# Optimization experiments

Hardware: AMD Instinct MI355X
Metric: run time of the kernel (lower is better)

The kernel has to match this reference:

```python
import jax, jax.numpy as jnp
import numpy as np

N_NODES = 50000
N_EDGES = 800000
IN_DIM = 128
HID = 256
OUT_DIM = 256
N_HEADS = 8
E_DIM = 64
KV_IN = 2 * IN_DIM + E_DIM  # 320


def _mlp_params(key, din, dhid, dout):
    k1, k2 = jax.random.split(key)
    s1 = 1.0 / np.sqrt(din)
    s2 = 1.0 / np.sqrt(dhid)
    return (jax.random.uniform(k1, (din, dhid), jnp.float32, -s1, s1),
            jnp.zeros((dhid,), jnp.float32),
            jax.random.uniform(k2, (dhid, dout), jnp.float32, -s2, s2),
            jnp.zeros((dout,), jnp.float32))


def setup_inputs() -> dict:
    key = jax.random.key(0)
    kh, ke, kidx, kk, kv, kq = jax.random.split(key, 6)
    h = jax.random.normal(kh, (N_NODES, IN_DIM), jnp.float32)
    e = jax.random.normal(ke, (N_EDGES, E_DIM), jnp.float32)
    edge_index = jax.random.randint(kidx, (2, N_EDGES), 0, N_NODES, jnp.int64)
    Wk1, bk1, Wk2, bk2 = _mlp_params(kk, KV_IN, HID, OUT_DIM)
    Wv1, bv1, Wv2, bv2 = _mlp_params(kv, KV_IN, HID, OUT_DIM)
    Wq1, bq1, Wq2, bq2 = _mlp_params(kq, IN_DIM, HID, OUT_DIM)
    return {"h": h, "e": e, "edge_index": edge_index,
            "Wk1": Wk1, "bk1": bk1, "Wk2": Wk2, "bk2": bk2,
            "Wv1": Wv1, "bv1": bv1, "Wv2": Wv2, "bv2": bv2,
            "Wq1": Wq1, "bq1": bq1, "Wq2": Wq2, "bq2": bq2}


def _mlp(x, W1, b1, W2, b2):
    # MLP(in, out, hidden, norm=False): Linear -> ReLU -> Linear
    return jax.nn.relu(x @ W1 + b1) @ W2 + b2


def reference(h, e, edge_index,
              Wk1, bk1, Wk2, bk2,
              Wv1, bv1, Wv2, bv2,
              Wq1, bq1, Wq2, bq2):
    N = h.shape[0]
    d_head = OUT_DIM // N_HEADS
    src, dst = edge_index[0], edge_index[1]
    # gather endpoints: hi = h[dst], hj = h[src]
    kv_input = jnp.concatenate([e, h[dst], h[src]], axis=-1)  # [E, KV_IN]
    k = _mlp(kv_input, Wk1, bk1, Wk2, bk2).reshape(-1, N_HEADS, d_head)
    v = _mlp(kv_input, Wv1, bv1, Wv2, bv2).reshape(-1, N_HEADS, d_head)
    q = _mlp(h, Wq1, bq1, Wq2, bq2).reshape(-1, N_HEADS, d_head)
    # per-edge logits, scaled dot product [E, H]
    logits = jnp.sum(q[dst] * k, axis=-1) * (1.0 / np.sqrt(d_head))
    # scatter softmax over destination groups
    mx = jax.ops.segment_max(logits, dst, num_segments=N)  # [N, H]
    ex = jnp.exp(logits - mx[dst])
    den = jax.ops.segment_sum(ex, dst, num_segments=N)  # [N, H]
    alpha = ex / den[dst]  # [E, H]
    # weighted scatter-sum aggregate
    m = alpha[..., None] * v  # [E, H, d_head]
    out = jax.ops.segment_sum(m, dst, num_segments=N)  # [N, H, d_head]
    return out.reshape(N, OUT_DIM)
```

## Files before the change

### kernel.cpp

```cpp
#include <hip/hip_runtime.h>

#define NND 50000
#define NE  800000
#define IND 128
#define HD  256
#define OD  256
#define NH  8
#define ED  64

typedef __attribute__((ext_vector_type(8))) short bf16x8;
typedef __attribute__((ext_vector_type(4))) float f32x4;

__device__ __forceinline__ float bf2f(unsigned short u) {
    union { unsigned int i; float f; } x; x.i = ((unsigned int)u) << 16; return x.f;
}
__device__ __forceinline__ unsigned short f2bf(float f) {
    union { float f; unsigned int i; } x; x.f = f;
    unsigned int u = x.i;
    u += 0x7FFFu + ((u >> 16) & 1u);
    return (unsigned short)(u >> 16);
}
__device__ __forceinline__ unsigned int pk2(float a, float b) {
    return (unsigned int)f2bf(a) | ((unsigned int)f2bf(b) << 16);
}

__global__ void k_hist(const int* __restrict__ eidx, int* __restrict__ cnt) {
    int e = blockIdx.x * 256 + threadIdx.x;
    if (e < NE) atomicAdd(&cnt[eidx[NE + e]], 1);
}

__global__ __launch_bounds__(1024) void k_scan(const int* __restrict__ cnt,
                                               int* __restrict__ head) {
    __shared__ int part[1024];
    const int t = threadIdx.x;
    const int CH = (NND + 1023) / 1024;
    int base = t * CH;
    int s = 0;
    for (int i = 0; i < CH; ++i) { int idx = base + i; if (idx < NND) s += cnt[idx]; }
    part[t] = s;
    __syncthreads();
    for (int off = 1; off < 1024; off <<= 1) {
        int v = (t >= off) ? part[t - off] : 0;
        __syncthreads();
        part[t] += v;
        __syncthreads();
    }
    int excl = (t == 0) ? 0 : part[t - 1];
    for (int i = 0; i < CH; ++i) {
        int idx = base + i; if (idx >= NND) break;
        head[idx] = excl;
        excl += cnt[idx];
    }
}

__global__ void k_scatter(const int* __restrict__ eidx, int* __restrict__ head,
                          int* __restrict__ perm, int* __restrict__ srcS,
                          int* __restrict__ dstS) {
    int e = blockIdx.x * 256 + threadIdx.x;
    if (e < NE) {
        int s = eidx[e];
        int d = eidx[NE + e];
        int pos = atomicAdd(&head[d], 1);
        perm[pos] = e;
        srcS[pos] = s;
        dstS[pos] = d;
    }
}

__global__ void k_eperm(const float* __restrict__ eattr, const int* __restrict__ perm,
                        unsigned short* __restrict__ ebf) {
    int i = blockIdx.x * 256 + threadIdx.x;
    if (i >= NE * 16) return;
    int pos = i >> 4, j = i & 15;
    int eid = perm[pos];
    float4 v = *(const float4*)(eattr + (size_t)eid * ED + j * 4);
    ushort4 o; o.x = f2bf(v.x); o.y = f2bf(v.y); o.z = f2bf(v.z); o.w = f2bf(v.w);
    *(ushort4*)(ebf + (size_t)pos * ED + j * 4) = o;
}

__global__ void k_packw(const float* __restrict__ W, unsigned short* __restrict__ P,
                        int K, int N, int rowoff) {
    int tid = blockIdx.x * 256 + threadIdx.x;
    if (tid >= K * N) return;
    int j = tid & 7;
    int l = (tid >> 3) & 63;
    int rest = tid >> 9;
    int KS = K >> 5;
    int ks = rest % KS;
    int ct = rest / KS;
    int n = ct * 16 + (l & 15);
    int k = ks * 32 + (l >> 4) * 8 + j;
    P[tid] = f2bf(W[(size_t)(rowoff + k) * N + n]);
}

__device__ __forceinline__ void zero_acc(f32x4 (&acc)[4][4]) {
    #pragma unroll
    for (int c = 0; c < 4; ++c)
        #pragma unroll
        for (int i = 0; i < 4; ++i)
            #pragma unroll
            for (int r = 0; r < 4; ++r) acc[c][i][r] = 0.f;
}

template<int KS, int STRIDE>
__device__ __forceinline__ void gemmT(const unsigned short* X,
                                      const unsigned short* __restrict__ Wp,
                                      int w, int l, f32x4 (&acc)[4][4]) {
    for (int ks = 0; ks < KS; ++ks) {
        bf16x8 wf[4], xf[4];
        #pragma unroll
        for (int c = 0; c < 4; ++c)
            wf[c] = *(const bf16x8*)(Wp + (((4 * w + c) * KS + ks) * 64 + l) * 8);
        #pragma unroll
        for (int i = 0; i < 4; ++i)
            xf[i] = *(const bf16x8*)(X + (i * 16 + (l & 15)) * STRIDE + ks * 32 + (l >> 4) * 8);
        #pragma unroll
        for (int c = 0; c < 4; ++c)
            #pragma unroll
            for (int i = 0; i < 4; ++i)
                acc[c][i] = __builtin_amdgcn_mfma_f32_16x16x32_bf16(wf[c], xf[i], acc[c][i], 0, 0, 0);
    }
}

__device__ __forceinline__ void lin_epi(const unsigned short* __restrict__ Wp,
                                        unsigned short* __restrict__ outp,
                                        const unsigned short* sXp,
                                        int w, int l, int g, int el, int m0) {
    f32x4 acc[4][4];
    zero_acc(acc);
    gemmT<4, 136>(sXp, Wp, w, l, acc);
    #pragma unroll
    for (int c = 0; c < 4; ++c) {
        int hid0 = 64 * w + 16 * c + 4 * g;
        #pragma unroll
        for (int i = 0; i < 4; ++i) {
            int node = m0 + 16 * i + el;
            if (node < NND) {
                uint2 pk;
                pk.x = pk2(acc[c][i][0], acc[c][i][1]);
                pk.y = pk2(acc[c][i][2], acc[c][i][3]);
                *(uint2*)(outp + (size_t)node * HD + hid0) = pk;
            }
        }
    }
}

__global__ __launch_bounds__(256) void k_node(
    const float* __restrict__ h,
    const unsigned short* __restrict__ Wq1p, const float* __restrict__ bq1,
    const unsigned short* __restrict__ Wq2p, const float* __restrict__ bq2,
    unsigned short* __restrict__ qb,
    const unsigned short* __restrict__ WdK, const unsigned short* __restrict__ WsK,
    const unsigned short* __restrict__ WdV, const unsigned short* __restrict__ WsV,
    unsigned short* __restrict__ udK, unsigned short* __restrict__ usK,
    unsigned short* __restrict__ udV, unsigned short* __restrict__ usV)
{
    __shared__ unsigned short sX[64][136];
    __shared__ unsigned short sH[64][264];
    const int t = threadIdx.x, w = t >> 6, l = t & 63;
    const int g = l >> 4, el = l & 15;
    const int m0 = blockIdx.x * 64;

    for (int c = t; c < 2048; c += 256) {
        int row = c >> 5, j = c & 31;
        int node = m0 + row; if (node >= NND) node = NND - 1;
        float4 v = *(const float4*)(h + (size_t)node * IND + j * 4);
        ushort4 o; o.x = f2bf(v.x); o.y = f2bf(v.y); o.z = f2bf(v.z); o.w = f2bf(v.w);
        *(ushort4*)(&sX[row][j * 4]) = o;
    }
    __syncthreads();

    f32x4 acc[4][4];
    zero_acc(acc);
    gemmT<4, 136>(&sX[0][0], Wq1p, w, l, acc);
    #pragma unroll
    for (int c = 0; c < 4; ++c) {
        int hid0 = 64 * w + 16 * c + 4 * g;
        float4 bv = *(const float4*)(bq1 + hid0);
        #pragma unroll
        for (int i = 0; i < 4; ++i) {
            uint2 pk;
            pk.x = pk2(fmaxf(acc[c][i][0] + bv.x, 0.f), fmaxf(acc[c][i][1] + bv.y, 0.f));
            pk.y = pk2(fmaxf(acc[c][i][2] + bv.z, 0.f), fmaxf(acc[c][i][3] + bv.w, 0.f));
            *(uint2*)(&sH[16 * i + el][hid0]) = pk;
        }
    }
    __syncthreads();

    zero_acc(acc);
    gemmT<8, 264>(&sH[0][0], Wq2p, w, l, acc);
    #pragma unroll
    for (int c = 0; c < 4; ++c) {
        int out0 = 64 * w + 16 * c + 4 * g;
        float4 bv = *(const float4*)(bq2 + out0);
        #pragma unroll
        for (int i = 0; i < 4; ++i) {
            int node = m0 + 16 * i + el;
            if (node < NND) {
                uint2 pk;
                pk.x = pk2(acc[c][i][0] + bv.x, acc[c][i][1] + bv.y);
                pk.y = pk2(acc[c][i][2] + bv.z, acc[c][i][3] + bv.w);
                *(uint2*)(qb + (size_t)node * OD + out0) = pk;
            }
        }
    }

    lin_epi(WdK, udK, &sX[0][0], w, l, g, el, m0);
    lin_epi(WsK, usK, &sX[0][0], w, l, g, el, m0);
    lin_epi(WdV, udV, &sX[0][0], w, l, g, el, m0);
    lin_epi(WsV, usV, &sX[0][0], w, l, g, el, m0);
}

struct SmF {
    unsigned short E[64][72];
    unsigned short H[64][264];
    int   Src[64];
    int   Dst[64];
    float Ex[64][8];
};

__device__ __forceinline__ void epi_pre(SmF& sm, f32x4 (&acc)[4][4],
                                        const float* __restrict__ b1,
                                        int w, int g, int el) {
    #pragma unroll
    for (int c = 0; c < 4; ++c) {
        int hid0 = 64 * w + 16 * c + 4 * g;
        float4 bv = *(const float4*)(b1 + hid0);
        #pragma unroll
        for (int i = 0; i < 4; ++i) {
            uint2 pk;
            pk.x = pk2(acc[c][i][0] + bv.x, acc[c][i][1] + bv.y);
            pk.y = pk2(acc[c][i][2] + bv.z, acc[c][i][3] + bv.w);
            *(uint2*)(&sm.H[16 * i + el][hid0]) = pk;
        }
    }
}

__device__ __forceinline__ void elemwise(SmF& sm,
                                         const unsigned short* __restrict__ ud,
                                         const unsigned short* __restrict__ us,
                                         int t) {
    int er = t >> 2;
    const unsigned short* udr = ud + (size_t)sm.Dst[er] * HD;
    const unsigned short* usr = us + (size_t)sm.Src[er] * HD;
    bf16x8 vd[8], vs[8];
    #pragma unroll
    for (int j = 0; j < 8; ++j) {
        int col = (j * 4 + (t & 3)) * 8;
        vd[j] = *(const bf16x8*)(udr + col);
        vs[j] = *(const bf16x8*)(usr + col);
    }
    #pragma unroll
    for (int j = 0; j < 8; ++j) {
        int col = (j * 4 + (t & 3)) * 8;
        bf16x8 hv = *(const bf16x8*)(&sm.H[er][col]);
        bf16x8 o;
        #pragma unroll
        for (int u = 0; u < 8; ++u) {
            float x = bf2f((unsigned short)hv[u]) + bf2f((unsigned short)vd[j][u])
                    + bf2f((unsigned short)vs[j][u]);
            o[u] = (short)f2bf(x > 0.f ? x : 0.f);
        }
        *(bf16x8*)(&sm.H[er][col]) = o;
    }
}

template<int PRE>
__global__ __launch_bounds__(256, 3) void k_edgeF(
    const float* __restrict__ eattr, const unsigned short* __restrict__ ebf,
    const int* __restrict__ perm,
    const int* __restrict__ srcS, const int* __restrict__ dstS,
    const unsigned short* __restrict__ WeK, const float* __restrict__ b1K,
    const unsigned short* __restrict__ W2K, const float* __restrict__ b2K,
    const unsigned short* __restrict__ WeV, const float* __restrict__ b1V,
    const unsigned short* __restrict__ W2V, const float* __restrict__ b2V,
    const unsigned short* __restrict__ udK, const unsigned short* __restrict__ usK,
    const unsigned short* __restrict__ udV, const unsigned short* __restrict__ usV,
    const unsigned short* __restrict__ qb,
    float* __restrict__ den, float* __restrict__ outp)
{
    __shared__ SmF sm;
    const int t = threadIdx.x, w = t >> 6, l = t & 63;
    const int g = l >> 4, el = l & 15;
    const int e0 = blockIdx.x * 64;

    if (t < 64) { sm.Src[t] = srcS[e0 + t]; sm.Dst[t] = dstS[e0 + t]; }
    if (PRE) {
        for (int c = t; c < 512; c += 256) {
            int row = c >> 3, j = c & 7;
            *(bf16x8*)(&sm.E[row][j * 8]) =
                *(const bf16x8*)(ebf + (size_t)(e0 + row) * ED + j * 8);
        }
    } else {
        for (int c = t; c < 1024; c += 256) {
            int row = c >> 4, j = c & 15;
            int eid = perm[e0 + row];
            float4 v = *(const float4*)(eattr + (size_t)eid * ED + j * 4);
            ushort4 o; o.x = f2bf(v.x); o.y = f2bf(v.y); o.z = f2bf(v.z); o.w = f2bf(v.w);
            *(ushort4*)(&sm.E[row][j * 4]) = o;
        }
    }
    __syncthreads();

    f32x4 acc[4][4];

    zero_acc(acc);
    gemmT<2, 72>(&sm.E[0][0], WeK, w, l, acc);
    epi_pre(sm, acc, b1K, w, g, el);
    __syncthreads();
    elemwise(sm, udK, usK, t);
    __syncthreads();

    zero_acc(acc);
    gemmT<8, 264>(&sm.H[0][0], W2K, w, l, acc);
    __syncthreads();
    epi_pre(sm, acc, b2K, w, g, el);
    __syncthreads();

    const float scale = 0.17677669529663687f;
    for (int p = t; p < 512; p += 256) {
        int er = p >> 3, hh = p & 7;
        const unsigned short* qrow = qb + (size_t)sm.Dst[er] * OD + hh * 32;
        float s = 0.f;
        #pragma unroll
        for (int jj = 0; jj < 32; jj += 8) {
            bf16x8 qv = *(const bf16x8*)(qrow + jj);
            bf16x8 kv = *(const bf16x8*)(&sm.H[er][hh * 32 + jj]);
            #pragma unroll
            for (int u = 0; u < 8; ++u)
                s += bf2f((unsigned short)qv[u]) * bf2f((unsigned short)kv[u]);
        }
        sm.Ex[er][hh] = __expf(s * scale);
    }
    __syncthreads();
    if (t < NH) {
        float run = 0.f; int prev = sm.Dst[0];
        for (int er = 0; er < 64; ++er) {
            int dn = sm.Dst[er];
            if (dn != prev) { atomicAdd(&den[prev * NH + t], run); run = 0.f; prev = dn; }
            run += sm.Ex[er][t];
        }
        atomicAdd(&den[prev * NH + t], run);
    }
    __syncthreads();

    zero_acc(acc);
    gemmT<2, 72>(&sm.E[0][0], WeV, w, l, acc);
    epi_pre(sm, acc, b1V, w, g, el);
    __syncthreads();
    elemwise(sm, udV, usV, t);
    __syncthreads();

    zero_acc(acc);
    gemmT<8, 264>(&sm.H[0][0], W2V, w, l, acc);
    __syncthreads();

    #pragma unroll
    for (int c = 0; c < 4; ++c) {
        int out0 = 64 * w + 16 * c + 4 * g;
        float4 bv = *(const float4*)(b2V + out0);
        int hh = out0 >> 5;
        #pragma unroll
        for (int i = 0; i < 4; ++i) {
            int edge = 16 * i + el;
            float ex = sm.Ex[edge][hh];
            uint2 pk;
            pk.x = pk2((acc[c][i][0] + bv.x) * ex, (acc[c][i][1] + bv.y) * ex);
            pk.y = pk2((acc[c][i][2] + bv.z) * ex, (acc[c][i][3] + bv.w) * ex);
            *(uint2*)(&sm.H[edge][out0]) = pk;
        }
    }
    __syncthreads();

    {
        float run = 0.f; int prev = sm.Dst[0];
        for (int er = 0; er < 64; ++er) {
            int dn = sm.Dst[er];
            if (dn != prev) {
                atomicAdd(outp + (size_t)prev * OD + t, run);
                run = 0.f; prev = dn;
            }
            run += bf2f(sm.H[er][t]);
        }
        atomicAdd(outp + (size_t)prev * OD + t, run);
    }
}

__global__ void k_norm(float* __restrict__ outp, const float* __restrict__ den) {
    int i = blockIdx.x * 256 + threadIdx.x;
    if (i >= NND * OD / 4) return;
    int node = i >> 6;
    int c4 = i & 63;
    int hh = (c4 >> 3);
    float inv = 1.f / den[node * NH + hh];
    float4 v = *(float4*)(outp + (size_t)i * 4);
    v.x *= inv; v.y *= inv; v.z *= inv; v.w *= inv;
    *(float4*)(outp + (size_t)i * 4) = v;
}

extern "C" void kernel_launch(void* const* d_in, const int* in_sizes, int n_in,
                              void* d_out, int out_size, void* d_ws, size_t ws_size,
                              hipStream_t stream)
{
    const float* h   = (const float*)d_in[0];
    const float* e   = (const float*)d_in[1];
    const int*   eid = (const int*)  d_in[2];
    const float* Wk1 = (const float*)d_in[3];
    const float* bk1 = (const float*)d_in[4];
    const float* Wk2 = (const float*)d_in[5];
    const float* bk2 = (const float*)d_in[6];
    const float* Wv1 = (const float*)d_in[7];
    const float* bv1 = (const float*)d_in[8];
    const float* Wv2 = (const float*)d_in[9];
    const float* bv2 = (const float*)d_in[10];
    const float* Wq1 = (const float*)d_in[11];
    const float* bq1 = (const float*)d_in[12];
    const float* Wq2 = (const float*)d_in[13];
    const float* bq2 = (const float*)d_in[14];

    char* ws = (char*)d_ws;
    size_t off = 0;
    auto take = [&](size_t bytes) { char* p = ws + off; off += bytes; return p; };
    unsigned short* qb   = (unsigned short*)take(25600000);
    unsigned short* udK  = (unsigned short*)take(25600000);
    unsigned short* usK  = (unsigned short*)take(25600000);
    unsigned short* udV  = (unsigned short*)take(25600000);
    unsigned short* usV  = (unsigned short*)take(25600000);
    float*          den  = (float*)         take(1600000);
    int*            cnt  = (int*)           take(200000);
    int*            head = (int*)           take(200000);
    int*            perm = (int*)           take(3200000);
    int*            srcS = (int*)           take(3200000);
    int*            dstS = (int*)           take(3200000);
    unsigned short* Wq1p = (unsigned short*)take(65536);
    unsigned short* Wq2p = (unsigned short*)take(131072);
    unsigned short* WeK  = (unsigned short*)take(32768);
    unsigned short* W2K  = (unsigned short*)take(131072);
    unsigned short* WdK  = (unsigned short*)take(65536);
    unsigned short* WsK  = (unsigned short*)take(65536);
    unsigned short* WeV  = (unsigned short*)take(32768);
    unsigned short* W2V  = (unsigned short*)take(131072);
    unsigned short* WdV  = (unsigned short*)take(65536);
    unsigned short* WsV  = (unsigned short*)take(65536);
    const size_t needed_small = off;
    unsigned short* ebf  = (unsigned short*)take((size_t)NE * ED * 2);
    const size_t needed_full = off;

    if (ws_size < needed_small) return;
    const bool pre = (ws_size >= needed_full);

    hipMemsetAsync(d_out, 0, (size_t)NND * OD * sizeof(float), stream);
    hipMemsetAsync(den, 0, (size_t)NND * NH * sizeof(float), stream);
    hipMemsetAsync(cnt, 0, (size_t)NND * sizeof(int), stream);

    k_hist<<<(NE + 255) / 256, 256, 0, stream>>>(eid, cnt);
    k_scan<<<1, 1024, 0, stream>>>(cnt, head);
    k_scatter<<<(NE + 255) / 256, 256, 0, stream>>>(eid, head, perm, srcS, dstS);

    k_packw<<<(IND * HD + 255) / 256, 256, 0, stream>>>(Wq1, Wq1p, IND, HD, 0);
    k_packw<<<(HD * OD + 255) / 256, 256, 0, stream>>>(Wq2, Wq2p, HD, OD, 0);
    k_packw<<<(ED * HD + 255) / 256, 256, 0, stream>>>(Wk1, WeK, ED, HD, 0);
    k_packw<<<(HD * OD + 255) / 256, 256, 0, stream>>>(Wk2, W2K, HD, OD, 0);
    k_packw<<<(IND * HD + 255) / 256, 256, 0, stream>>>(Wk1, WdK, IND, HD, 64);
    k_packw<<<(IND * HD + 255) / 256, 256, 0, stream>>>(Wk1, WsK, IND, HD, 192);
    k_packw<<<(ED * HD + 255) / 256, 256, 0, stream>>>(Wv1, WeV, ED, HD, 0);
    k_packw<<<(HD * OD + 255) / 256, 256, 0, stream>>>(Wv2, W2V, HD, OD, 0);
    k_packw<<<(IND * HD + 255) / 256, 256, 0, stream>>>(Wv1, WdV, IND, HD, 64);
    k_packw<<<(IND * HD + 255) / 256, 256, 0, stream>>>(Wv1, WsV, IND, HD, 192);

    if (pre)
        k_eperm<<<(NE * 16 + 255) / 256, 256, 0, stream>>>(e, perm, ebf);

    k_node<<<(NND + 63) / 64, 256, 0, stream>>>(h, Wq1p, bq1, Wq2p, bq2, qb,
                                                WdK, WsK, WdV, WsV,
                                                udK, usK, udV, usV);

    if (pre)
        k_edgeF<1><<<NE / 64, 256, 0, stream>>>(e, ebf, perm, srcS, dstS,
                                                WeK, bk1, W2K, bk2,
                                                WeV, bv1, W2V, bv2,
                                                udK, usK, udV, usV,
                                                qb, den, (float*)d_out);
    else
        k_edgeF<0><<<NE / 64, 256, 0, stream>>>(e, ebf, perm, srcS, dstS,
                                                WeK, bk1, W2K, bk2,
                                                WeV, bv1, W2V, bv2,
                                                udK, usK, udV, usV,
                                                qb, den, (float*)d_out);

    k_norm<<<(NND * OD / 4 + 255) / 256, 256, 0, stream>>>((float*)d_out, den);
}
```

Baseline: 902.5 us.

## Drop edge-attr pre-permute kernel, use hardware bf16 pack, repad LDS strides

Removes the separate k_eperm pass and always gathers edge attributes in fp32 inside the edge kernel, converting them to bf16 in-kernel. Edge ids are staged in shared memory first, which adds one barrier. Float-to-bf16 packing now uses the v_cvt_pk_bf16_f32 instruction instead of a software rounding sequence. LDS row strides change from 72/136/264 to 80/144/272 elements, presumably to alter bank-conflict behaviour. The norm kernel also guards against zero denominators.

Measured after the change: 861.0 us. 4.6% less time.

```diff
diff --git a/kernel.cpp b/kernel.cpp
--- a/kernel.cpp
+++ b/kernel.cpp
@@ -21,7 +21,9 @@
     return (unsigned short)(u >> 16);
 }
 __device__ __forceinline__ unsigned int pk2(float a, float b) {
-    return (unsigned int)f2bf(a) | ((unsigned int)f2bf(b) << 16);
+    unsigned int r;
+    asm("v_cvt_pk_bf16_f32 %0, %1, %2" : "=v"(r) : "v"(a), "v"(b));
+    return r;
 }
 
 __global__ void k_hist(const int* __restrict__ eidx, int* __restrict__ cnt) {
@@ -65,17 +67,6 @@
         srcS[pos] = s;
         dstS[pos] = d;
     }
-}
-
-__global__ void k_eperm(const float* __restrict__ eattr, const int* __restrict__ perm,
-                        unsigned short* __restrict__ ebf) {
-    int i = blockIdx.x * 256 + threadIdx.x;
-    if (i >= NE * 16) return;
-    int pos = i >> 4, j = i & 15;
-    int eid = perm[pos];
-    float4 v = *(const float4*)(eattr + (size_t)eid * ED + j * 4);
-    ushort4 o; o.x = f2bf(v.x); o.y = f2bf(v.y); o.z = f2bf(v.z); o.w = f2bf(v.w);
-    *(ushort4*)(ebf + (size_t)pos * ED + j * 4) = o;
 }
 
 __global__ void k_packw(const float* __restrict__ W, unsigned short* __restrict__ P,
@@ -128,7 +119,7 @@
                                         int w, int l, int g, int el, int m0) {
     f32x4 acc[4][4];
     zero_acc(acc);
-    gemmT<4, 136>(sXp, Wp, w, l, acc);
+    gemmT<4, 144>(sXp, Wp, w, l, acc);
     #pragma unroll
     for (int c = 0; c < 4; ++c) {
         int hid0 = 64 * w + 16 * c + 4 * g;
@@ -155,8 +146,8 @@
     unsigned short* __restrict__ udK, unsigned short* __restrict__ usK,
     unsigned short* __restrict__ udV, unsigned short* __restrict__ usV)
 {
-    __shared__ unsigned short sX[64][136];
-    __shared__ unsigned short sH[64][264];
+    __shared__ unsigned short sX[64][144];
+    __shared__ unsigned short sH[64][272];
     const int t = threadIdx.x, w = t >> 6, l = t & 63;
     const int g = l >> 4, el = l & 15;
     const int m0 = blockIdx.x * 64;
@@ -165,14 +156,14 @@
         int row = c >> 5, j = c & 31;
         int node = m0 + row; if (node >= NND) node = NND - 1;
         float4 v = *(const float4*)(h + (size_t)node * IND + j * 4);
-        ushort4 o; o.x = f2bf(v.x); o.y = f2bf(v.y); o.z = f2bf(v.z); o.w = f2bf(v.w);
-        *(ushort4*)(&sX[row][j * 4]) = o;
+        uint2 pk; pk.x = pk2(v.x, v.y); pk.y = pk2(v.z, v.w);
+        *(uint2*)(&sX[row][j * 4]) = pk;
     }
     __syncthreads();
 
     f32x4 acc[4][4];
     zero_acc(acc);
-    gemmT<4, 136>(&sX[0][0], Wq1p, w, l, acc);
+    gemmT<4, 144>(&sX[0][0], Wq1p, w, l, acc);
     #pragma unroll
     for (int c = 0; c < 4; ++c) {
         int hid0 = 64 * w + 16 * c + 4 * g;
@@ -188,7 +179,7 @@
     __syncthreads();
 
     zero_acc(acc);
-    gemmT<8, 264>(&sH[0][0], Wq2p, w, l, acc);
+    gemmT<8, 272>(&sH[0][0], Wq2p, w, l, acc);
     #pragma unroll
     for (int c = 0; c < 4; ++c) {
         int out0 = 64 * w + 16 * c + 4 * g;
@@ -212,8 +203,9 @@
 }
 
 struct SmF {
-    unsigned short E[64][72];
-    unsigned short H[64][264];
+    unsigned short E[64][80];
+    unsigned short H[64][272];
+    int   Eid[64];
     int   Src[64];
     int   Dst[64];
     float Ex[64][8];
@@ -254,20 +246,22 @@
     for (int j = 0; j < 8; ++j) {
         int col = (j * 4 + (t & 3)) * 8;
         bf16x8 hv = *(const bf16x8*)(&sm.H[er][col]);
-        bf16x8 o;
+        float x[8];
         #pragma unroll
         for (int u = 0; u < 8; ++u) {
-            float x = bf2f((unsigned short)hv[u]) + bf2f((unsigned short)vd[j][u])
-                    + bf2f((unsigned short)vs[j][u]);
-            o[u] = (short)f2bf(x > 0.f ? x : 0.f);
-        }
-        *(bf16x8*)(&sm.H[er][col]) = o;
-    }
-}
-
-template<int PRE>
+            x[u] = bf2f((unsigned short)hv[u]) + bf2f((unsigned short)vd[j][u])
+                 + bf2f((unsigned short)vs[j][u]);
+            x[u] = fmaxf(x[u], 0.f);
+        }
+        uint4 o;
+        o.x = pk2(x[0], x[1]); o.y = pk2(x[2], x[3]);
+        o.z = pk2(x[4], x[5]); o.w = pk2(x[6], x[7]);
+        *(uint4*)(&sm.H[er][col]) = o;
+    }
+}
+
 __global__ __launch_bounds__(256, 3) void k_edgeF(
-    const float* __restrict__ eattr, const unsigned short* __restrict__ ebf,
+    const float* __restrict__ eattr,
     const int* __restrict__ perm,
     const int* __restrict__ srcS, const int* __restrict__ dstS,
     const unsigned short* __restrict__ WeK, const float* __restrict__ b1K,
@@ -284,35 +278,31 @@
     const int g = l >> 4, el = l & 15;
     const int e0 = blockIdx.x * 64;
 
-    if (t < 64) { sm.Src[t] = srcS[e0 + t]; sm.Dst[t] = dstS[e0 + t]; }
-    if (PRE) {
-        for (int c = t; c < 512; c += 256) {
-            int row = c >> 3, j = c & 7;
-            *(bf16x8*)(&sm.E[row][j * 8]) =
-                *(const bf16x8*)(ebf + (size_t)(e0 + row) * ED + j * 8);
-        }
-    } else {
-        for (int c = t; c < 1024; c += 256) {
-            int row = c >> 4, j = c & 15;
-            int eid = perm[e0 + row];
-            float4 v = *(const float4*)(eattr + (size_t)eid * ED + j * 4);
-            ushort4 o; o.x = f2bf(v.x); o.y = f2bf(v.y); o.z = f2bf(v.z); o.w = f2bf(v.w);
-            *(ushort4*)(&sm.E[row][j * 4]) = o;
-        }
+    if (t < 64) {
+        sm.Eid[t] = perm[e0 + t];
+        sm.Src[t] = srcS[e0 + t];
+        sm.Dst[t] = dstS[e0 + t];
+    }
+    __syncthreads();
+    for (int c = t; c < 1024; c += 256) {
+        int row = c >> 4, j = c & 15;
+        float4 v = *(const float4*)(eattr + (size_t)sm.Eid[row] * ED + j * 4);
+        uint2 pk; pk.x = pk2(v.x, v.y); pk.y = pk2(v.z, v.w);
+        *(uint2*)(&sm.E[row][j * 4]) = pk;
     }
     __syncthreads();
 
     f32x4 acc[4][4];
 
     zero_acc(acc);
-    gemmT<2, 72>(&sm.E[0][0], WeK, w, l, acc);
+    gemmT<2, 80>(&sm.E[0][0], WeK, w, l, acc);
     epi_pre(sm, acc, b1K, w, g, el);
     __syncthreads();
     elemwise(sm, udK, usK, t);
     __syncthreads();
 
     zero_acc(acc);
-    gemmT<8, 264>(&sm.H[0][0], W2K, w, l, acc);
+    gemmT<8, 272>(&sm.H[0][0], W2K, w, l, acc);
     __syncthreads();
     epi_pre(sm, acc, b2K, w, g, el);
     __syncthreads();
@@ -345,14 +335,14 @@
     __syncthreads();
 
     zero_acc(acc);
-    gemmT<2, 72>(&sm.E[0][0], WeV, w, l, acc);
+    gemmT<2, 80>(&sm.E[0][0], WeV, w, l, acc);
     epi_pre(sm, acc, b1V, w, g, el);
     __syncthreads();
     elemwise(sm, udV, usV, t);
     __syncthreads();
 
     zero_acc(acc);
-    gemmT<8, 264>(&sm.H[0][0], W2V, w, l, acc);
+    gemmT<8, 272>(&sm.H[0][0], W2V, w, l, acc);
     __syncthreads();
 
     #pragma unroll
@@ -392,7 +382,8 @@
     int node = i >> 6;
     int c4 = i & 63;
     int hh = (c4 >> 3);
-    float inv = 1.f / den[node * NH + hh];
+    float d = den[node * NH + hh];
+    float inv = d > 0.f ? 1.f / d : 0.f;
     float4 v = *(float4*)(outp + (size_t)i * 4);
     v.x *= inv; v.y *= inv; v.z *= inv; v.w *= inv;
     *(float4*)(outp + (size_t)i * 4) = v;
@@ -442,12 +433,8 @@
     unsigned short* W2V  = (unsigned short*)take(131072);
     unsigned short* WdV  = (unsigned short*)take(65536);
     unsigned short* WsV  = (unsigned short*)take(65536);
-    const size_t needed_small = off;
-    unsigned short* ebf  = (unsigned short*)take((size_t)NE * ED * 2);
-    const size_t needed_full = off;
-
-    if (ws_size < needed_small) return;
-    const bool pre = (ws_size >= needed_full);
+    const size_t needed = off;
+    if (ws_size < needed) return;
 
     hipMemsetAsync(d_out, 0, (size_t)NND * OD * sizeof(float), stream);
     hipMemsetAsync(den, 0, (size_t)NND * NH * sizeof(float), stream);
@@ -468,25 +455,15 @@
     k_packw<<<(IND * HD + 255) / 256, 256, 0, stream>>>(Wv1, WdV, IND, HD, 64);
     k_packw<<<(IND * HD + 255) / 256, 256, 0, stream>>>(Wv1, WsV, IND, HD, 192);
 
-    if (pre)
-        k_eperm<<<(NE * 16 + 255) / 256, 256, 0, stream>>>(e, perm, ebf);
-
     k_node<<<(NND + 63) / 64, 256, 0, stream>>>(h, Wq1p, bq1, Wq2p, bq2, qb,
                                                 WdK, WsK, WdV, WsV,
                                                 udK, usK, udV, usV);
 
-    if (pre)
-        k_edgeF<1><<<NE / 64, 256, 0, stream>>>(e, ebf, perm, srcS, dstS,
-                                                WeK, bk1, W2K, bk2,
-                                                WeV, bv1, W2V, bv2,
-                                                udK, usK, udV, usV,
-                                                qb, den, (float*)d_out);
-    else
-        k_edgeF<0><<<NE / 64, 256, 0, stream>>>(e, ebf, perm, srcS, dstS,
-                                                WeK, bk1, W2K, bk2,
-                                                WeV, bv1, W2V, bv2,
-                                                udK, usK, udV, usV,
-                                                qb, den, (float*)d_out);
+    k_edgeF<<<NE / 64, 256, 0, stream>>>(e, perm, srcS, dstS,
+                                         WeK, bk1, W2K, bk2,
+                                         WeV, bv1, W2V, bv2,
+                                         udK, usK, udV, usV,
+                                         qb, den, (float*)d_out);
 
     k_norm<<<(NND * OD / 4 + 255) / 256, 256, 0, stream>>>((float*)d_out, den);
 }
```
